# Kernel optimization log

Hardware: AMD Instinct MI355X
Metric: run time of the kernel (lower is better)

The kernel has to match this reference:

```python
import jax, jax.numpy as jnp
import numpy as np

N = 100000      # nodes
E = 1600000     # directed edges (avg degree 16)
D_IN = 64
D_OUT = 64


def setup_inputs() -> dict:
    key = jax.random.key(0)
    k1, k2, k3, k4, k5 = jax.random.split(key, 5)
    x = jax.random.normal(k1, (N, D_IN), dtype=jnp.float32)
    edge_index = jax.random.randint(k2, (2, E), 0, N, dtype=jnp.int32)
    s_in = 1.0 / np.sqrt(D_IN)
    W_conv = jax.random.normal(k3, (D_IN, D_OUT), dtype=jnp.float32) * s_in
    b_conv = jnp.zeros((D_OUT,), dtype=jnp.float32)
    W_self = jax.random.normal(k4, (D_IN, D_OUT), dtype=jnp.float32) * s_in
    b_self = jax.random.normal(k5, (D_OUT,), dtype=jnp.float32) * s_in
    return {"x": x, "edge_index": edge_index, "W_conv": W_conv, "b_conv": b_conv,
            "W_self": W_self, "b_self": b_self, "n1": 400, "n2": 250}


def reference(x, edge_index, W_conv, b_conv, W_self, b_self, n1, n2):
    # GCNConv (PyG defaults): add self-loops, symmetric normalization,
    # out_i = sum_j norm_ij * (x_j @ W_conv) + b_conv; then self-loop linear + residual.
    n = x.shape[0]
    loops = jnp.arange(n, dtype=edge_index.dtype)
    row = jnp.concatenate([edge_index[0], loops])  # source nodes [E+N]
    col = jnp.concatenate([edge_index[1], loops])  # target nodes [E+N]
    deg = jax.ops.segment_sum(jnp.ones_like(col, dtype=x.dtype), col, num_segments=n)
    dinv = jnp.where(deg > 0, jax.lax.rsqrt(deg), 0.0)      # deg^{-1/2}
    norm = dinv[row] * dinv[col]                            # [E+N]
    xw = x @ W_conv                                         # [N, D_OUT]
    msg = xw[row] * norm[:, None]                           # gather + scale [E+N, D_OUT]
    x_neigh = jax.ops.segment_sum(msg, col, num_segments=n) + b_conv
    x_self = x @ W_self + b_self
    return x_self + x_neigh
```

## Files before the change

kernel.cpp:

```cpp
#include <hip/hip_runtime.h>

#define CAP 64
#define CHUNK 4096
#define NBINS_MAX 1024
#define CAPB 2560

typedef __attribute__((ext_vector_type(8))) short bf16x8;
typedef __attribute__((ext_vector_type(4))) float f32x4;

__device__ __forceinline__ unsigned short f2bf_rne(float f) {
    unsigned u = __builtin_bit_cast(unsigned, f);
    u += 0x7FFFu + ((u >> 16) & 1u);
    return (unsigned short)(u >> 16);
}
__device__ __forceinline__ float bf2f(unsigned short h) {
    return __builtin_bit_cast(float, (unsigned)h << 16);
}


__global__ void k_zero2(int* __restrict__ gcur, int nbins, int* __restrict__ degovf,
                        int n, int* __restrict__ ovfc,
                        const float* __restrict__ Wc, const float* __restrict__ Ws,
                        unsigned short* __restrict__ bfrag) {
    const int t = threadIdx.x;
    if (blockIdx.x == gridDim.x - 1) {
        for (int s = t; s < 2048; s += 256) {
            int lane = s & 63;
            int ct   = (s >> 6) & 3;
            int ks   = (s >> 8) & 1;
            int half = (s >> 9) & 1;
            int mat  = (s >> 10) & 1;
            const float* W = mat ? Ws : Wc;
            int d = ct * 16 + (lane & 15);
            int kbase = ks * 32 + (lane >> 4) * 8;
#pragma unroll
            for (int j = 0; j < 8; ++j) {
                float v = W[(kbase + j) * 64 + d];
                unsigned u = __builtin_bit_cast(unsigned, v);
                unsigned short hi = (unsigned short)(u >> 16);
                unsigned short elem;
                if (half == 0) {
                    elem = hi;
                } else {
                    float fh = __builtin_bit_cast(float, (unsigned)hi << 16);
                    float fl = v - fh;
                    elem = (unsigned short)(__builtin_bit_cast(unsigned, fl) >> 16);
                }
                bfrag[(size_t)s * 8 + j] = elem;
            }
        }
        return;
    }
    int i = blockIdx.x * blockDim.x + t;
    if (i < nbins) gcur[i] = 0;
    if (i < n) degovf[i] = 0;
    if (i == 0) *ovfc = 0;
}

__global__ __launch_bounds__(512) void k_bin(
    const int* __restrict__ row, const int* __restrict__ col, int e, int nbins,
    int* __restrict__ gcur, unsigned int* __restrict__ records,
    int* __restrict__ degovf, int* __restrict__ ovf, int* __restrict__ ovfc)
{
    __shared__ int hist[NBINS_MAX];
    __shared__ int lofs[NBINS_MAX];
    __shared__ int gadj[NBINS_MAX];
    __shared__ int tscan[512];
    __shared__ unsigned int stage[CHUNK];
    __shared__ unsigned short sbin[CHUNK];

    const int t = threadIdx.x;
    const int base = blockIdx.x * CHUNK;
    int cnt = e - base; if (cnt > CHUNK) cnt = CHUNK;
    if (cnt <= 0) return;

    for (int i = t; i < nbins; i += 512) hist[i] = 0;
    __syncthreads();

    for (int k = t; k < cnt; k += 512) atomicAdd(&hist[col[base + k] >> 7], 1);
    __syncthreads();

    const int b0 = t * 2;
    int h0 = (b0 < nbins) ? hist[b0] : 0;
    int h1 = (b0 + 1 < nbins) ? hist[b0 + 1] : 0;
    int s = h0 + h1;
    tscan[t] = s;
    __syncthreads();
    for (int off = 1; off < 512; off <<= 1) {
        int v = (t >= off) ? tscan[t - off] : 0;
        __syncthreads();
        tscan[t] += v;
        __syncthreads();
    }
    const int tbase = tscan[t] - s;

    if (b0 < nbins) {
        int gb = h0 ? atomicAdd(&gcur[b0], h0) : 0;
        lofs[b0] = tbase; gadj[b0] = gb - tbase;
    }
    if (b0 + 1 < nbins) {
        int lb = tbase + h0;
        int gb = h1 ? atomicAdd(&gcur[b0 + 1], h1) : 0;
        lofs[b0 + 1] = lb; gadj[b0 + 1] = gb - lb;
    }
    __syncthreads();

    for (int k = t; k < cnt; k += 512) {
        int c = col[base + k];
        int r = row[base + k];
        int b = c >> 7;
        int slot = atomicAdd(&lofs[b], 1);
        stage[slot] = ((unsigned)r << 7) | (unsigned)(c & 127);
        sbin[slot] = (unsigned short)b;
    }
    __syncthreads();

    for (int k = t; k < cnt; k += 512) {
        unsigned rec = stage[k];
        int b = sbin[k];
        int g = gadj[b] + k;
        if (g < CAPB) {
            records[(size_t)b * CAPB + g] = rec;
        } else {
            int q = atomicAdd(ovfc, 1);
            int c = (b << 7) | (int)(rec & 127u);
            ovf[2 * q]     = (int)(rec >> 7);
            ovf[2 * q + 1] = c;
            atomicAdd(&degovf[c], 1);
        }
    }
}

__global__ __launch_bounds__(256) void k_xprep(
    const float* __restrict__ x, const unsigned int* __restrict__ records,
    const int* __restrict__ gcur, const int* __restrict__ degovf,
    float* __restrict__ dinv, unsigned short* __restrict__ xbf, int n)
{
    __shared__ int lh[128];
    __shared__ float sdinv[128];
    const int b = blockIdx.x, t = threadIdx.x;

    if (t < 128) lh[t] = 0;
    __syncthreads();
    int m = gcur[b]; if (m > CAPB) m = CAPB;
    const unsigned int* rb = records + (size_t)b * CAPB;
    for (int k = t; k < m; k += 256) atomicAdd(&lh[rb[k] & 127u], 1);
    __syncthreads();
    if (t < 128) {
        int node = (b << 7) + t;
        int dov = (node < n) ? degovf[node] : 0;
        float v = rsqrtf((float)(lh[t] + dov + 1));
        sdinv[t] = v;
        if (node < n) dinv[node] = v;
    }
    __syncthreads();

#pragma unroll
    for (int i = 0; i < 4; ++i) {
        int pos = t + i * 256;
        int node = (b << 7) + (pos >> 3);
        if (node >= n) break;
        float dv = sdinv[pos >> 3];
        const float4* xp = (const float4*)(x + (size_t)b * 8192 + (size_t)pos * 8);
        float4 f0 = xp[0], f1 = xp[1];
        uint4 u;
        u.x = (unsigned)f2bf_rne(f0.x * dv) | ((unsigned)f2bf_rne(f0.y * dv) << 16);
        u.y = (unsigned)f2bf_rne(f0.z * dv) | ((unsigned)f2bf_rne(f0.w * dv) << 16);
        u.z = (unsigned)f2bf_rne(f1.x * dv) | ((unsigned)f2bf_rne(f1.y * dv) << 16);
        u.w = (unsigned)f2bf_rne(f1.z * dv) | ((unsigned)f2bf_rne(f1.w * dv) << 16);
        *(uint4*)(xbf + (size_t)b * 8192 + (size_t)pos * 8) = u;
    }
}

__global__ __launch_bounds__(512) void k_agg(
    const int* __restrict__ gcur, const unsigned int* __restrict__ records,
    const unsigned short* __restrict__ xbf, unsigned short* __restrict__ agg, int n)
{
    __shared__ unsigned int srec[CAPB];
    __shared__ int slist[CAPB];
    __shared__ int scnt[128];
    __shared__ int sinc[128];
    __shared__ int scur[128];

    const int b = blockIdx.x, t = threadIdx.x;
    int m = gcur[b]; if (m > CAPB) m = CAPB;

    if (t < 128) scnt[t] = 0;
    __syncthreads();

    for (int k = t; k < m; k += 512) {
        unsigned r = __builtin_nontemporal_load(&records[(size_t)b * CAPB + k]);
        srec[k] = r;
        atomicAdd(&scnt[r & 127u], 1);
    }
    __syncthreads();

    if (t < 128) sinc[t] = scnt[t];
    __syncthreads();
    for (int off = 1; off < 128; off <<= 1) {
        int v = 0;
        if (t < 128 && t >= off) v = sinc[t - off];
        __syncthreads();
        if (t < 128) sinc[t] += v;
        __syncthreads();
    }
    if (t < 128) scur[t] = sinc[t] - scnt[t];
    __syncthreads();

    for (int k = t; k < m; k += 512) {
        unsigned r = srec[k];
        int slot = atomicAdd(&scur[r & 127u], 1);
        slist[slot] = (int)(r & ~127u);
    }
    __syncthreads();

    const int wave = t >> 6, lane = t & 63;
    const int h = lane >> 5;
    const char* ybl = (const char*)xbf + ((lane & 31) << 2);

    for (int i = wave; i < 128; i += 8) {
        int node = (b << 7) + i;
        if (node >= n) break;
        int cnt = scnt[i];
        int beg = sinc[i] - cnt;
        float ax0=0.f,ax1=0.f,ax2=0.f,ax3=0.f,ax4=0.f,ax5=0.f,ax6=0.f,ax7=0.f;
        float ay0=0.f,ay1=0.f,ay2=0.f,ay3=0.f,ay4=0.f,ay5=0.f,ay6=0.f,ay7=0.f;
        int k = 0;
        for (; k + 16 <= cnt; k += 16) {
            int o0 = slist[beg + k + 0  + h];
            int o1 = slist[beg + k + 2  + h];
            int o2 = slist[beg + k + 4  + h];
            int o3 = slist[beg + k + 6  + h];
            int o4 = slist[beg + k + 8  + h];
            int o5 = slist[beg + k + 10 + h];
            int o6 = slist[beg + k + 12 + h];
            int o7 = slist[beg + k + 14 + h];
            unsigned v0 = *(const unsigned*)(ybl + o0);
            unsigned v1 = *(const unsigned*)(ybl + o1);
            unsigned v2 = *(const unsigned*)(ybl + o2);
            unsigned v3 = *(const unsigned*)(ybl + o3);
            unsigned v4 = *(const unsigned*)(ybl + o4);
            unsigned v5 = *(const unsigned*)(ybl + o5);
            unsigned v6 = *(const unsigned*)(ybl + o6);
            unsigned v7 = *(const unsigned*)(ybl + o7);
            ax0 += bf2f((unsigned short)v0); ay0 += bf2f((unsigned short)(v0 >> 16));
            ax1 += bf2f((unsigned short)v1); ay1 += bf2f((unsigned short)(v1 >> 16));
            ax2 += bf2f((unsigned short)v2); ay2 += bf2f((unsigned short)(v2 >> 16));
            ax3 += bf2f((unsigned short)v3); ay3 += bf2f((unsigned short)(v3 >> 16));
            ax4 += bf2f((unsigned short)v4); ay4 += bf2f((unsigned short)(v4 >> 16));
            ax5 += bf2f((unsigned short)v5); ay5 += bf2f((unsigned short)(v5 >> 16));
            ax6 += bf2f((unsigned short)v6); ay6 += bf2f((unsigned short)(v6 >> 16));
            ax7 += bf2f((unsigned short)v7); ay7 += bf2f((unsigned short)(v7 >> 16));
        }
        for (; k + 2 <= cnt; k += 2) {
            int o = slist[beg + k + h];
            unsigned v = *(const unsigned*)(ybl + o);
            ax0 += bf2f((unsigned short)v);
            ay0 += bf2f((unsigned short)(v >> 16));
        }
        if (k < cnt && h == 0) {
            int o = slist[beg + k];
            unsigned v = *(const unsigned*)(ybl + o);
            ax0 += bf2f((unsigned short)v);
            ay0 += bf2f((unsigned short)(v >> 16));
        }
        float sx = ((ax0+ax1)+(ax2+ax3)) + ((ax4+ax5)+(ax6+ax7));
        float sy = ((ay0+ay1)+(ay2+ay3)) + ((ay4+ay5)+(ay6+ay7));
        sx += __shfl_down(sx, 32);
        sy += __shfl_down(sy, 32);
        if (h == 0) {
            unsigned own = *(const unsigned*)((const char*)xbf + ((size_t)node << 7) + ((lane & 31) << 2));
            sx += bf2f((unsigned short)own);
            sy += bf2f((unsigned short)(own >> 16));
            unsigned pk = (unsigned)f2bf_rne(sx) | ((unsigned)f2bf_rne(sy) << 16);
            __builtin_nontemporal_store(pk,
                (unsigned*)((char*)agg + ((size_t)node << 7) + ((lane & 31) << 2)));
        }
    }
}

__global__ __launch_bounds__(256) void k_gemm7(
    const float* __restrict__ x, const unsigned short* __restrict__ aggbf,
    const unsigned short* __restrict__ bfrag, const float* __restrict__ bc,
    const float* __restrict__ bs, const float* __restrict__ dinv,
    float* __restrict__ out, int n)
{
    __shared__ float sdinv[128];
    const int b = blockIdx.x;
    const int t = threadIdx.x;
    if (t < 128) {
        int node = (b << 7) + t;
        sdinv[t] = (node < n) ? dinv[node] : 0.f;
    }
    __syncthreads();

    const int lane = t & 63;
    const int wid = t >> 6;
    const int rt0 = b * 128 + wid * 32;
    const int lbase = wid * 32;
    if (rt0 >= n) return;

    const int arow = lane & 15;
    const int kgrp = lane >> 4;

    bf16x8 a_x[2][2], a_g[2][2];
#pragma unroll
    for (int rt = 0; rt < 2; ++rt) {
        int row = rt0 + rt * 16 + arow;
        if (row >= n) row = n - 1;
        const float* xp = x + (size_t)row * 64 + kgrp * 8;
#pragma unroll
        for (int ks = 0; ks < 2; ++ks) {
            float4 f0 = *(const float4*)(xp + ks * 32);
            float4 f1 = *(const float4*)(xp + ks * 32 + 4);
            float f[8] = {f0.x, f0.y, f0.z, f0.w, f1.x, f1.y, f1.z, f1.w};
            bf16x8 hh;
#pragma unroll
            for (int j = 0; j < 8; ++j) {
                unsigned u = __builtin_bit_cast(unsigned, f[j]);
                hh[j] = (short)(unsigned short)(u >> 16);
            }
            a_x[rt][ks] = hh;
            a_g[rt][ks] = *(const bf16x8*)(aggbf + (size_t)row * 64 + ks * 32 + kgrp * 8);
        }
    }

    f32x4 acc[2][2][4];
#pragma unroll
    for (int mm = 0; mm < 2; ++mm)
#pragma unroll
        for (int rt = 0; rt < 2; ++rt)
#pragma unroll
            for (int ct = 0; ct < 4; ++ct)
                acc[mm][rt][ct] = (f32x4){0.f, 0.f, 0.f, 0.f};

#pragma unroll
    for (int mat = 0; mat < 2; ++mat) {
#pragma unroll
        for (int ks = 0; ks < 2; ++ks) {
#pragma unroll
            for (int ct = 0; ct < 4; ++ct) {
                const bf16x8 bh = *(const bf16x8*)(bfrag + ((size_t)((((mat * 2 + 0) * 2 + ks) * 4 + ct) * 64 + lane)) * 8);
                const bf16x8 bl = *(const bf16x8*)(bfrag + ((size_t)((((mat * 2 + 1) * 2 + ks) * 4 + ct) * 64 + lane)) * 8);
#pragma unroll
                for (int rt = 0; rt < 2; ++rt) {
                    bf16x8 A = (mat == 0) ? a_g[rt][ks] : a_x[rt][ks];
                    acc[mat][rt][ct] = __builtin_amdgcn_mfma_f32_16x16x32_bf16(A, bh, acc[mat][rt][ct], 0, 0, 0);
                    acc[mat][rt][ct] = __builtin_amdgcn_mfma_f32_16x16x32_bf16(A, bl, acc[mat][rt][ct], 0, 0, 0);
                }
            }
        }
    }

    const int dcol = lane & 15;
    const int rbase = (lane >> 4) * 4;
    float di[2][4];
#pragma unroll
    for (int rt = 0; rt < 2; ++rt)
#pragma unroll
        for (int reg = 0; reg < 4; ++reg)
            di[rt][reg] = sdinv[lbase + rt * 16 + rbase + reg];

#pragma unroll
    for (int ct = 0; ct < 4; ++ct) {
        int d = ct * 16 + dcol;
        float bias = bc[d] + bs[d];
#pragma unroll
        for (int rt = 0; rt < 2; ++rt) {
#pragma unroll
            for (int reg = 0; reg < 4; ++reg) {
                int row = rt0 + rt * 16 + rbase + reg;
                if (row < n) {
                    out[(size_t)row * 64 + d] =
                        acc[1][rt][ct][reg] + bias + di[rt][reg] * acc[0][rt][ct][reg];
                }
            }
        }
    }
}

__global__ void k_ovf3(const int* __restrict__ ovfc, const int* __restrict__ ovf,
                       const float* __restrict__ dinv, const unsigned short* __restrict__ xbf,
                       const float* __restrict__ Wc, float* __restrict__ out) {
    int m = *ovfc;
    int wid = (blockIdx.x * blockDim.x + threadIdx.x) >> 6;
    int lane = threadIdx.x & 63;
    int nw = (gridDim.x * blockDim.x) >> 6;
    for (int q = wid; q < m; q += nw) {
        int r = ovf[2 * q], c = ovf[2 * q + 1];
        float acc = 0.f;
        for (int k = 0; k < 64; ++k)
            acc += bf2f(xbf[(size_t)r * 64 + k]) * Wc[k * 64 + lane];
        unsafeAtomicAdd(out + (size_t)c * 64 + lane, dinv[c] * acc);
    }
}


__global__ void k_init(int* __restrict__ cnt, int* __restrict__ ovf_cnt, int n) {
    int i = blockIdx.x * blockDim.x + threadIdx.x;
    if (i < n) cnt[i] = 0;
    if (i == 0) *ovf_cnt = 0;
}

__global__ void k_fill_pad(const int* __restrict__ row, const int* __restrict__ col,
                           int* __restrict__ cnt, int* __restrict__ bucket,
                           int* __restrict__ ovf, int* __restrict__ ovf_cnt, int e) {
    int i = blockIdx.x * blockDim.x + threadIdx.x;
    if (i >= e) return;
    int c = col[i];
    int p = atomicAdd(&cnt[c], 1);
    if (p < CAP) bucket[(size_t)c * CAP + p] = row[i];
    else { int q = atomicAdd(ovf_cnt, 1); ovf[q] = i; }
}

__global__ __launch_bounds__(256) void k_gemm(
    const float* __restrict__ x, const float* __restrict__ Wc,
    const float* __restrict__ bc, const float* __restrict__ Ws,
    const float* __restrict__ bs, const int* __restrict__ deg, int add,
    float* __restrict__ dinv, float* __restrict__ y,
    float* __restrict__ out, int n)
{
    __shared__ __align__(16) float sWc[64 * 64];
    __shared__ __align__(16) float sWs[64 * 64];
    __shared__ __align__(16) float sx[64 * 64];
    const int t = threadIdx.x;

    for (int i = t; i < 1024; i += 256) {
        ((float4*)sWc)[i] = ((const float4*)Wc)[i];
        ((float4*)sWs)[i] = ((const float4*)Ws)[i];
    }
    const int row0 = blockIdx.x * 64;
    int nrows = n - row0; if (nrows > 64) nrows = 64;
    for (int i = t; i < nrows * 16; i += 256) {
        ((float4*)sx)[i] = ((const float4*)(x + (size_t)row0 * 64))[i];
    }
    __syncthreads();

    const int d = t & 63;
    const int g = t >> 6;

    float wcr[64], wsr[64];
#pragma unroll
    for (int k = 0; k < 64; ++k) { wcr[k] = sWc[k * 64 + d]; wsr[k] = sWs[k * 64 + d]; }

    const float bcd = bc[d], bsd = bs[d];

    for (int rr = g * 16; rr < (g + 1) * 16; ++rr) {
        if (rr >= nrows) break;
        float accC = 0.f, accS = 0.f;
        const float4* xv4 = (const float4*)(sx + rr * 64);
#pragma unroll
        for (int q = 0; q < 16; ++q) {
            float4 xv = xv4[q];
            accC += xv.x*wcr[4*q+0] + xv.y*wcr[4*q+1] + xv.z*wcr[4*q+2] + xv.w*wcr[4*q+3];
            accS += xv.x*wsr[4*q+0] + xv.y*wsr[4*q+1] + xv.z*wsr[4*q+2] + xv.w*wsr[4*q+3];
        }
        const int r = row0 + rr;
        const float di = rsqrtf((float)(deg[r] + add));
        if (d == 0) dinv[r] = di;
        const float yv = accC * di;
        y[(size_t)r * 64 + d] = yv;
        out[(size_t)r * 64 + d] = accS + bsd + bcd + di * yv;
    }
}

__global__ __launch_bounds__(256) void k_gather_pad(
    const int* __restrict__ cnt, const int* __restrict__ bucket,
    const float* __restrict__ y, float* __restrict__ out, int n)
{
    const int node = blockIdx.x * 4 + (threadIdx.x >> 6);
    if (node >= n) return;
    const int lane = threadIdx.x & 63;
    int m = cnt[node];
    const float di = rsqrtf((float)(m + 1));
    if (m > CAP) m = CAP;
    if (m == 0) return;

    int rl = (lane < m) ? bucket[(size_t)node * CAP + lane] : 0;

    float a0=0.f,a1=0.f,a2=0.f,a3=0.f,a4=0.f,a5=0.f,a6=0.f,a7=0.f;
    int k = 0;
    for (; k + 8 <= m; k += 8) {
        int r0=__shfl(rl,k+0), r1=__shfl(rl,k+1), r2=__shfl(rl,k+2), r3=__shfl(rl,k+3);
        int r4=__shfl(rl,k+4), r5=__shfl(rl,k+5), r6=__shfl(rl,k+6), r7=__shfl(rl,k+7);
        a0 += y[(size_t)r0*64 + lane];
        a1 += y[(size_t)r1*64 + lane];
        a2 += y[(size_t)r2*64 + lane];
        a3 += y[(size_t)r3*64 + lane];
        a4 += y[(size_t)r4*64 + lane];
        a5 += y[(size_t)r5*64 + lane];
        a6 += y[(size_t)r6*64 + lane];
        a7 += y[(size_t)r7*64 + lane];
    }
    for (; k + 2 <= m; k += 2) {
        int r0=__shfl(rl,k+0), r1=__shfl(rl,k+1);
        a0 += y[(size_t)r0*64 + lane];
        a1 += y[(size_t)r1*64 + lane];
    }
    if (k < m) { int r0=__shfl(rl,k); a0 += y[(size_t)r0*64 + lane]; }

    float acc = ((a0+a1)+(a2+a3)) + ((a4+a5)+(a6+a7));
    out[(size_t)node*64 + lane] += di * acc;
}

__global__ void k_ovf_idx(const int* __restrict__ ovf_cnt, const int* __restrict__ ovf,
                          const int* __restrict__ row, const int* __restrict__ col,
                          const float* __restrict__ dinv, const float* __restrict__ y,
                          float* __restrict__ out) {
    int m = *ovf_cnt;
    long long total = (long long)m * 16;
    for (long long idx = blockIdx.x*blockDim.x+threadIdx.x; idx < total;
         idx += (long long)gridDim.x*blockDim.x) {
        int ei = ovf[idx >> 4];
        int j = (int)(idx & 15);
        int r = row[ei], c = col[ei];
        float s = dinv[c];
        float4 v = ((const float4*)y)[(size_t)r*16 + j];
        float* o = out + (size_t)c*64 + (j<<2);
        unsafeAtomicAdd(o+0, s*v.x);
        unsafeAtomicAdd(o+1, s*v.y);
        unsafeAtomicAdd(o+2, s*v.z);
        unsafeAtomicAdd(o+3, s*v.w);
    }
}

__global__ void k_deg_init(int* __restrict__ deg, int n) {
    int i = blockIdx.x * blockDim.x + threadIdx.x;
    if (i < n) deg[i] = 1;
}

__global__ void k_deg_count(const int* __restrict__ col, int* __restrict__ deg, int e) {
    int i = blockIdx.x * blockDim.x + threadIdx.x;
    if (i < e) atomicAdd(&deg[col[i]], 1);
}

__global__ __launch_bounds__(256) void k_scatter(
    const int* __restrict__ row, const int* __restrict__ col,
    const float* __restrict__ dinv, const float* __restrict__ y,
    float* __restrict__ out, int e)
{
    int idx = blockIdx.x * blockDim.x + threadIdx.x;
    int eidx = idx >> 4;
    if (eidx >= e) return;
    int j = idx & 15;
    int r = row[eidx];
    int c = col[eidx];
    float s = dinv[c];
    float4 v = ((const float4*)y)[(size_t)r * 16 + j];
    float* o = out + (size_t)c * 64 + (j << 2);
    unsafeAtomicAdd(o + 0, s * v.x);
    unsafeAtomicAdd(o + 1, s * v.y);
    unsafeAtomicAdd(o + 2, s * v.z);
    unsafeAtomicAdd(o + 3, s * v.w);
}

extern "C" void kernel_launch(void* const* d_in, const int* in_sizes, int n_in,
                              void* d_out, int out_size, void* d_ws, size_t ws_size,
                              hipStream_t stream) {
    const float* x  = (const float*)d_in[0];
    const int*   ei = (const int*)d_in[1];
    const float* Wc = (const float*)d_in[2];
    const float* bc = (const float*)d_in[3];
    const float* Ws = (const float*)d_in[4];
    const float* bs = (const float*)d_in[5];
    float* out = (float*)d_out;

    const int n = in_sizes[0] / 64;
    const int e = in_sizes[1] / 2;
    const int* rowi = ei;
    const int* coli = ei + e;

    auto align = [](size_t v) { return (v + 255) & ~(size_t)255; };
    char* ws = (char*)d_ws;
    const int nbins = (n + 127) >> 7;

    size_t m_dinv = 0;
    size_t m_xbf  = align(m_dinv + (size_t)n * 4);
    size_t m_agg  = align(m_xbf  + (size_t)n * 128);
    size_t m_gcur = align(m_agg  + (size_t)n * 128);
    size_t m_rec  = align(m_gcur + (size_t)nbins * 4);
    size_t m_dov  = align(m_rec  + (size_t)nbins * CAPB * 4);
    size_t m_ovf  = align(m_dov  + (size_t)n * 4);
    size_t m_ovfc = align(m_ovf  + (size_t)e * 8);
    size_t m_bfr  = align(m_ovfc + 256);
    size_t m_tot  = m_bfr + 32768;

    size_t p_cnt  = 0;
    size_t p_dinv = align(p_cnt  + (size_t)n * 4);
    size_t p_y    = align(p_dinv + (size_t)n * 4);
    size_t p_bkt  = align(p_y    + (size_t)n * 256);
    size_t p_ovf  = align(p_bkt  + (size_t)n * CAP * 4);
    size_t p_ovfc = align(p_ovf  + (size_t)e * 4);
    size_t p_tot  = p_ovfc + 256;

    if (nbins <= NBINS_MAX && m_tot <= ws_size) {
        float* dinv = (float*)(ws + m_dinv);
        unsigned short* xbf = (unsigned short*)(ws + m_xbf);
        unsigned short* agg = (unsigned short*)(ws + m_agg);
        int*   gcur = (int*)(ws + m_gcur);
        unsigned int* rec = (unsigned int*)(ws + m_rec);
        int*   dov  = (int*)(ws + m_dov);
        int*   ovf  = (int*)(ws + m_ovf);
        int*   ovfc = (int*)(ws + m_ovfc);
        unsigned short* bfrag = (unsigned short*)(ws + m_bfr);

        int zmax = (n > nbins) ? n : nbins;
        k_zero2<<<(zmax + 255) / 256 + 1, 256, 0, stream>>>(gcur, nbins, dov, n, ovfc,
                                                            Wc, Ws, bfrag);
        k_bin<<<(e + CHUNK - 1) / CHUNK, 512, 0, stream>>>(rowi, coli, e, nbins,
                                                           gcur, rec, dov, ovf, ovfc);
        k_xprep<<<nbins, 256, 0, stream>>>(x, rec, gcur, dov, dinv, xbf, n);
        k_agg<<<nbins, 512, 0, stream>>>(gcur, rec, xbf, agg, n);
        k_gemm7<<<nbins, 256, 0, stream>>>(x, agg, bfrag, bc, bs, dinv, out, n);
        k_ovf3<<<64, 256, 0, stream>>>(ovfc, ovf, dinv, xbf, Wc, out);
    } else if (p_tot <= ws_size) {
        int*   cnt    = (int*)(ws + p_cnt);
        float* dinv   = (float*)(ws + p_dinv);
        float* y      = (float*)(ws + p_y);
        int*   bucket = (int*)(ws + p_bkt);
        int*   ovf    = (int*)(ws + p_ovf);
        int*   ovfc   = (int*)(ws + p_ovfc);

        k_init<<<(n + 255) / 256, 256, 0, stream>>>(cnt, ovfc, n);
        k_fill_pad<<<(e + 255) / 256, 256, 0, stream>>>(rowi, coli, cnt, bucket, ovf, ovfc, e);
        k_gemm<<<(n + 63) / 64, 256, 0, stream>>>(x, Wc, bc, Ws, bs, cnt, 1, dinv, y, out, n);
        k_gather_pad<<<(n + 3) / 4, 256, 0, stream>>>(cnt, bucket, y, out, n);
        k_ovf_idx<<<64, 256, 0, stream>>>(ovfc, ovf, rowi, coli, dinv, y, out);
    } else {
        size_t a_deg  = 0;
        size_t a_dinv = align(a_deg  + (size_t)n * 4);
        size_t a_y    = align(a_dinv + (size_t)n * 4);
        int*   deg  = (int*)(ws + a_deg);
        float* dinv = (float*)(ws + a_dinv);
        float* y    = (float*)(ws + a_y);
        k_deg_init<<<(n + 255) / 256, 256, 0, stream>>>(deg, n);
        k_deg_count<<<(e + 255) / 256, 256, 0, stream>>>(coli, deg, e);
        k_gemm<<<(n + 63) / 64, 256, 0, stream>>>(x, Wc, bc, Ws, bs, deg, 0, dinv, y, out, n);
        long long tot = (long long)e * 16;
        k_scatter<<<(int)((tot + 255) / 256), 256, 0, stream>>>(rowi, coli, dinv, y, out, e);
    }
}
```

Before: 115.1 us.

## Fuse aggregation and dual GEMM into one kernel via shared-memory staging

Merges the neighbour-aggregation kernel and the MFMA GEMM kernel into one launch. The aggregated bf16 rows stay in a padded shared-memory tile instead of making a global round trip. The self term now reads the pre-scaled bf16 x and divides by dinv, instead of reloading fp32 x. This removes a kernel launch, the agg write and read, and the fp32 x read, but rescaling by 1/dinv changes rounding and the shared-memory footprint per block grows.

```diff
diff --git a/kernel.cpp b/kernel.cpp
--- a/kernel.cpp
+++ b/kernel.cpp
@@ -4,6 +4,7 @@
 #define CHUNK 4096
 #define NBINS_MAX 1024
 #define CAPB 2560
+#define AGG_STRIDE 72
 
 typedef __attribute__((ext_vector_type(8))) short bf16x8;
 typedef __attribute__((ext_vector_type(4))) float f32x4;
@@ -172,20 +173,29 @@
     }
 }
 
-__global__ __launch_bounds__(512) void k_agg(
+__global__ __launch_bounds__(512) void k_aggemm(
     const int* __restrict__ gcur, const unsigned int* __restrict__ records,
-    const unsigned short* __restrict__ xbf, unsigned short* __restrict__ agg, int n)
+    const unsigned short* __restrict__ xbf, const float* __restrict__ dinv,
+    const unsigned short* __restrict__ bfrag, const float* __restrict__ bc,
+    const float* __restrict__ bs, float* __restrict__ out, int n)
 {
-    __shared__ unsigned int srec[CAPB];
-    __shared__ int slist[CAPB];
-    __shared__ int scnt[128];
-    __shared__ int sinc[128];
-    __shared__ int scur[128];
+    __shared__ __align__(16) char smem[12288 + 128 * AGG_STRIDE * 2];
+    int* slist            = (int*)smem;
+    int* scnt             = (int*)(smem + 10240);
+    int* sinc             = (int*)(smem + 10752);
+    int* scur             = (int*)(smem + 11264);
+    float* sdinv          = (float*)(smem + 11776);
+    unsigned int* srec    = (unsigned int*)(smem + 12288);
+    unsigned short* sagg  = (unsigned short*)(smem + 12288);
 
     const int b = blockIdx.x, t = threadIdx.x;
     int m = gcur[b]; if (m > CAPB) m = CAPB;
 
-    if (t < 128) scnt[t] = 0;
+    if (t < 128) {
+        scnt[t] = 0;
+        int node = (b << 7) + t;
+        sdinv[t] = (node < n) ? dinv[node] : 1.0f;
+    }
     __syncthreads();
 
     for (int k = t; k < m; k += 512) {
@@ -273,107 +283,54 @@
             sx += bf2f((unsigned short)own);
             sy += bf2f((unsigned short)(own >> 16));
             unsigned pk = (unsigned)f2bf_rne(sx) | ((unsigned)f2bf_rne(sy) << 16);
-            __builtin_nontemporal_store(pk,
-                (unsigned*)((char*)agg + ((size_t)node << 7) + ((lane & 31) << 2)));
-        }
-    }
-}
-
-__global__ __launch_bounds__(256) void k_gemm7(
-    const float* __restrict__ x, const unsigned short* __restrict__ aggbf,
-    const unsigned short* __restrict__ bfrag, const float* __restrict__ bc,
-    const float* __restrict__ bs, const float* __restrict__ dinv,
-    float* __restrict__ out, int n)
-{
-    __shared__ float sdinv[128];
-    const int b = blockIdx.x;
-    const int t = threadIdx.x;
-    if (t < 128) {
-        int node = (b << 7) + t;
-        sdinv[t] = (node < n) ? dinv[node] : 0.f;
-    }
-    __syncthreads();
-
-    const int lane = t & 63;
-    const int wid = t >> 6;
-    const int rt0 = b * 128 + wid * 32;
-    const int lbase = wid * 32;
-    if (rt0 >= n) return;
+            ((unsigned*)sagg)[i * (AGG_STRIDE / 2) + (lane & 31)] = pk;
+        }
+    }
+    __syncthreads();
+
+    const int lrow0 = wave * 16;
+    const int grow0 = (b << 7) + lrow0;
+    if (grow0 >= n) return;
 
     const int arow = lane & 15;
     const int kgrp = lane >> 4;
-
-    bf16x8 a_x[2][2], a_g[2][2];
-#pragma unroll
-    for (int rt = 0; rt < 2; ++rt) {
-        int row = rt0 + rt * 16 + arow;
-        if (row >= n) row = n - 1;
-        const float* xp = x + (size_t)row * 64 + kgrp * 8;
+    int lrow = lrow0 + arow;
+    int grow = (b << 7) + lrow; if (grow >= n) grow = n - 1;
+
+    bf16x8 a_x[2], a_g[2];
+#pragma unroll
+    for (int ks = 0; ks < 2; ++ks) {
+        a_x[ks] = *(const bf16x8*)(xbf + (size_t)grow * 64 + ks * 32 + kgrp * 8);
+        a_g[ks] = *(const bf16x8*)(sagg + lrow * AGG_STRIDE + ks * 32 + kgrp * 8);
+    }
+
+    const int dcol = lane & 15;
+    const int rb2 = (lane >> 4) * 4;
+
+#pragma unroll
+    for (int ct = 0; ct < 4; ++ct) {
+        f32x4 accC = (f32x4){0.f, 0.f, 0.f, 0.f};
+        f32x4 accS = (f32x4){0.f, 0.f, 0.f, 0.f};
 #pragma unroll
         for (int ks = 0; ks < 2; ++ks) {
-            float4 f0 = *(const float4*)(xp + ks * 32);
-            float4 f1 = *(const float4*)(xp + ks * 32 + 4);
-            float f[8] = {f0.x, f0.y, f0.z, f0.w, f1.x, f1.y, f1.z, f1.w};
-            bf16x8 hh;
-#pragma unroll
-            for (int j = 0; j < 8; ++j) {
-                unsigned u = __builtin_bit_cast(unsigned, f[j]);
-                hh[j] = (short)(unsigned short)(u >> 16);
-            }
-            a_x[rt][ks] = hh;
-            a_g[rt][ks] = *(const bf16x8*)(aggbf + (size_t)row * 64 + ks * 32 + kgrp * 8);
-        }
-    }
-
-    f32x4 acc[2][2][4];
-#pragma unroll
-    for (int mm = 0; mm < 2; ++mm)
-#pragma unroll
-        for (int rt = 0; rt < 2; ++rt)
-#pragma unroll
-            for (int ct = 0; ct < 4; ++ct)
-                acc[mm][rt][ct] = (f32x4){0.f, 0.f, 0.f, 0.f};
-
-#pragma unroll
-    for (int mat = 0; mat < 2; ++mat) {
-#pragma unroll
-        for (int ks = 0; ks < 2; ++ks) {
-#pragma unroll
-            for (int ct = 0; ct < 4; ++ct) {
-                const bf16x8 bh = *(const bf16x8*)(bfrag + ((size_t)((((mat * 2 + 0) * 2 + ks) * 4 + ct) * 64 + lane)) * 8);
-                const bf16x8 bl = *(const bf16x8*)(bfrag + ((size_t)((((mat * 2 + 1) * 2 + ks) * 4 + ct) * 64 + lane)) * 8);
-#pragma unroll
-                for (int rt = 0; rt < 2; ++rt) {
-                    bf16x8 A = (mat == 0) ? a_g[rt][ks] : a_x[rt][ks];
-                    acc[mat][rt][ct] = __builtin_amdgcn_mfma_f32_16x16x32_bf16(A, bh, acc[mat][rt][ct], 0, 0, 0);
-                    acc[mat][rt][ct] = __builtin_amdgcn_mfma_f32_16x16x32_bf16(A, bl, acc[mat][rt][ct], 0, 0, 0);
-                }
-            }
-        }
-    }
-
-    const int dcol = lane & 15;
-    const int rbase = (lane >> 4) * 4;
-    float di[2][4];
-#pragma unroll
-    for (int rt = 0; rt < 2; ++rt)
-#pragma unroll
-        for (int reg = 0; reg < 4; ++reg)
-            di[rt][reg] = sdinv[lbase + rt * 16 + rbase + reg];
-
-#pragma unroll
-    for (int ct = 0; ct < 4; ++ct) {
+            const bf16x8 ch = *(const bf16x8*)(bfrag + ((size_t)(((0 * 2 + ks) * 4 + ct) * 64 + lane)) * 8);
+            const bf16x8 cl = *(const bf16x8*)(bfrag + ((size_t)(((1 * 2 + ks) * 4 + ct) * 64 + lane)) * 8);
+            accC = __builtin_amdgcn_mfma_f32_16x16x32_bf16(a_g[ks], ch, accC, 0, 0, 0);
+            accC = __builtin_amdgcn_mfma_f32_16x16x32_bf16(a_g[ks], cl, accC, 0, 0, 0);
+            const bf16x8 sh = *(const bf16x8*)(bfrag + ((size_t)(((2 * 2 + ks) * 4 + ct) * 64 + lane)) * 8);
+            const bf16x8 sl = *(const bf16x8*)(bfrag + ((size_t)(((3 * 2 + ks) * 4 + ct) * 64 + lane)) * 8);
+            accS = __builtin_amdgcn_mfma_f32_16x16x32_bf16(a_x[ks], sh, accS, 0, 0, 0);
+            accS = __builtin_amdgcn_mfma_f32_16x16x32_bf16(a_x[ks], sl, accS, 0, 0, 0);
+        }
         int d = ct * 16 + dcol;
         float bias = bc[d] + bs[d];
 #pragma unroll
-        for (int rt = 0; rt < 2; ++rt) {
-#pragma unroll
-            for (int reg = 0; reg < 4; ++reg) {
-                int row = rt0 + rt * 16 + rbase + reg;
-                if (row < n) {
-                    out[(size_t)row * 64 + d] =
-                        acc[1][rt][ct][reg] + bias + di[rt][reg] * acc[0][rt][ct][reg];
-                }
+        for (int reg = 0; reg < 4; ++reg) {
+            int lr = lrow0 + rb2 + reg;
+            int row = (b << 7) + lr;
+            if (row < n) {
+                float dv = sdinv[lr];
+                out[(size_t)row * 64 + d] = accS[reg] / dv + bias + dv * accC[reg];
             }
         }
     }
@@ -576,8 +533,7 @@
 
     size_t m_dinv = 0;
     size_t m_xbf  = align(m_dinv + (size_t)n * 4);
-    size_t m_agg  = align(m_xbf  + (size_t)n * 128);
-    size_t m_gcur = align(m_agg  + (size_t)n * 128);
+    size_t m_gcur = align(m_xbf  + (size_t)n * 128);
     size_t m_rec  = align(m_gcur + (size_t)nbins * 4);
     size_t m_dov  = align(m_rec  + (size_t)nbins * CAPB * 4);
     size_t m_ovf  = align(m_dov  + (size_t)n * 4);
@@ -596,7 +552,6 @@
     if (nbins <= NBINS_MAX && m_tot <= ws_size) {
         float* dinv = (float*)(ws + m_dinv);
         unsigned short* xbf = (unsigned short*)(ws + m_xbf);
-        unsigned short* agg = (unsigned short*)(ws + m_agg);
         int*   gcur = (int*)(ws + m_gcur);
         unsigned int* rec = (unsigned int*)(ws + m_rec);
         int*   dov  = (int*)(ws + m_dov);
@@ -610,8 +565,7 @@
         k_bin<<<(e + CHUNK - 1) / CHUNK, 512, 0, stream>>>(rowi, coli, e, nbins,
                                                            gcur, rec, dov, ovf, ovfc);
         k_xprep<<<nbins, 256, 0, stream>>>(x, rec, gcur, dov, dinv, xbf, n);
-        k_agg<<<nbins, 512, 0, stream>>>(gcur, rec, xbf, agg, n);
-        k_gemm7<<<nbins, 256, 0, stream>>>(x, agg, bfrag, bc, bs, dinv, out, n);
+        k_aggemm<<<nbins, 512, 0, stream>>>(gcur, rec, xbf, dinv, bfrag, bc, bs, out, n);
         k_ovf3<<<64, 256, 0, stream>>>(ovfc, ovf, dinv, xbf, Wc, out);
     } else if (p_tot <= ws_size) {
         int*   cnt    = (int*)(ws + p_cnt);
```

Result: slower. 142.7 us (+24.0%).
